# Kernel tuning notes

Measured on AMD Instinct MI355X. Metric: run time of the kernel, lower is better.

## Reference

```python
import jax, jax.numpy as jnp
import numpy as np

# Dimensions
T = 1024      # tokens
D = 1024      # d_model
DFF = 1024    # expert intermediate dim
R = 64        # tucker rank (r_in == r_out)
G = 8         # n_group
E = 32        # experts_per_group
NEXP = G * E  # 256 routed experts
K = 8         # top-k


def setup_inputs() -> dict:
    key = jax.random.key(0)
    ks = jax.random.split(key, 12)
    s = 0.02
    return {
        "x": jax.random.normal(ks[0], (T, D), jnp.float32),
        "Wg": jax.random.normal(ks[1], (D, NEXP), jnp.float32) * s,
        "uin_gate": jax.random.normal(ks[2], (G, D, R), jnp.float32) * s,
        "core_gate": jax.random.normal(ks[3], (G, E, R, R), jnp.float32) * s,
        "uout_gate": jax.random.normal(ks[4], (G, R, DFF), jnp.float32) * s,
        "uin_up": jax.random.normal(ks[5], (G, D, R), jnp.float32) * s,
        "core_up": jax.random.normal(ks[6], (G, E, R, R), jnp.float32) * s,
        "uout_up": jax.random.normal(ks[7], (G, R, DFF), jnp.float32) * s,
        "uin_down": jax.random.normal(ks[8], (G, DFF, R), jnp.float32) * s,
        "core_down": jax.random.normal(ks[9], (G, E, R, R), jnp.float32) * s,
        "uout_down": jax.random.normal(ks[10], (G, R, D), jnp.float32) * s,
    }


def _moe_forward(x, Wg, uin_gate, core_gate, uout_gate,
                 uin_up, core_up, uout_up,
                 uin_down, core_down, uout_down):
    Tn, d = x.shape
    # Router: top-k over 256 experts, softmax over the k logits (fp32 as in torch)
    logits = x @ Wg                                   # [T, NEXP]
    w, sel = jax.lax.top_k(logits, K)                 # [T, K]
    w = jax.nn.softmax(w.astype(jnp.float32), axis=-1).astype(x.dtype)

    e = sel.reshape(-1)                               # [F] global expert id
    g = e // E                                        # [F] group id
    tok = jnp.repeat(jnp.arange(Tn), K)               # [F] source token id
    mask = (g[:, None] == jnp.arange(G)[None, :]).astype(x.dtype)  # [F, G]

    def gather_in(uin):
        # project tokens with every group's u_in once, then gather per pair
        pre = jnp.einsum('td,gdr->gtr', x, uin)       # [G, T, R]
        return pre[g, tok]                            # [F, R]

    def core_apply(xin, core):
        # per-pair Tucker core slice bmm: x.unsqueeze(1) @ core[rel_idx]
        slices = core.reshape(G * E, R, R)[e]         # [F, R, R] gather
        return jnp.einsum('fr,fro->fo', xin, slices)  # [F, R]

    def group_out(h, U):
        # per-pair group-specific projection: h[f] @ U[g_f]
        out = jnp.zeros((h.shape[0], U.shape[-1]), h.dtype)
        for gi in range(G):  # fixed small loop over 8 groups
            out = out + (h * mask[:, gi:gi + 1]) @ U[gi]
        return out

    gate_h = group_out(core_apply(gather_in(uin_gate), core_gate), uout_gate)  # [F, DFF]
    up_h = group_out(core_apply(gather_in(uin_up), core_up), uout_up)          # [F, DFF]
    act = jax.nn.silu(gate_h) * up_h                                           # SwiGLU
    xin_d = group_out(act, uin_down)                                           # [F, R]
    out_f = group_out(core_apply(xin_d, core_down), uout_down)                 # [F, D]
    out_f = out_f * w.reshape(-1)[:, None]
    # scatter-add expert outputs back to tokens
    return jax.ops.segment_sum(out_f, tok, num_segments=Tn)


def reference(x, Wg, uin_gate, core_gate, uout_gate,
              uin_up, core_up, uout_up,
              uin_down, core_down, uout_down):
    return _moe_forward(x, Wg, uin_gate, core_gate, uout_gate,
                        uin_up, core_up, uout_up,
                        uin_down, core_down, uout_down)
```

## Files before the change

### kernel.cpp

```cpp
#include <hip/hip_runtime.h>
#include <hip/hip_bf16.h>
#include <math.h>


#define T_ 1024
#define D_ 1024
#define DFF_ 1024
#define R_ 64
#define G_ 8
#define E_ 32
#define NEXP_ 256
#define K_ 8
#define F_ 8192
#define LKZ_ 4
#define LTB_ 8
#define PKZ_ 2
#define DKZ_ 4

typedef short bf16x8 __attribute__((ext_vector_type(8)));
typedef float f32x4 __attribute__((ext_vector_type(4)));

__device__ __forceinline__ unsigned short f2bf(float f) {
  unsigned int u = __float_as_uint(f);
  u += 0x7fffu + ((u >> 16) & 1u);
  return (unsigned short)(u >> 16);
}

typedef const __attribute__((address_space(1))) unsigned int guint;
typedef __attribute__((address_space(3))) unsigned int luint;

__device__ __forceinline__ void gstage(short* lds, const unsigned short* src,
                                       int gp, int tid) {
  int w = tid >> 6, l = tid & 63;
  int r0 = (w << 4) + (l >> 3);
  int c = (l & 7) << 3;
  __builtin_amdgcn_global_load_lds((guint*)&src[(size_t)r0 * gp + c],
                                   (luint*)&lds[w << 10], 16, 0, 0);
  __builtin_amdgcn_global_load_lds((guint*)&src[(size_t)(r0 + 8) * gp + c],
                                   (luint*)&lds[(w << 10) + 512], 16, 0, 0);
}

__device__ __forceinline__ void gstage_clamp(short* lds, const unsigned short* src,
                                             int gp, int rows_valid, int tid) {
  int w = tid >> 6, l = tid & 63;
  int c = (l & 7) << 3;
  int r0 = (w << 4) + (l >> 3);
  int r1 = r0 + 8;
  if (r0 >= rows_valid) r0 = rows_valid - 1;
  if (r1 >= rows_valid) r1 = rows_valid - 1;
  __builtin_amdgcn_global_load_lds((guint*)&src[(size_t)r0 * gp + c],
                                   (luint*)&lds[w << 10], 16, 0, 0);
  __builtin_amdgcn_global_load_lds((guint*)&src[(size_t)r1 * gp + c],
                                   (luint*)&lds[(w << 10) + 512], 16, 0, 0);
}

__device__ __forceinline__ void mma_strip(const short* As, const short* Bs,
                                          int ms, int lane, f32x4* acc) {
  int lm = lane & 15;
  int lk = (lane >> 4) << 3;
#pragma unroll
  for (int kc = 0; kc < 64; kc += 32) {
    bf16x8 a = *(const bf16x8*)&As[(ms + lm) * 64 + kc + lk];
#pragma unroll
    for (int nt = 0; nt < 4; ++nt) {
      bf16x8 b = *(const bf16x8*)&Bs[(nt * 16 + lm) * 64 + kc + lk];
      acc[nt] = __builtin_amdgcn_mfma_f32_16x16x32_bf16(a, b, acc[nt], 0, 0, 0);
    }
  }
}

__device__ __forceinline__ void a_load(float4* pre, const float* src, int gp, int tid) {
  int r = tid >> 2, c = (tid & 3) << 4;
  const float* s = &src[(size_t)r * gp + c];
  pre[0] = *(const float4*)(s + 0);
  pre[1] = *(const float4*)(s + 4);
  pre[2] = *(const float4*)(s + 8);
  pre[3] = *(const float4*)(s + 12);
}

__device__ __forceinline__ void a_write(short* dst, const float4* pre, int tid) {
  int r = tid >> 2, c = (tid & 3) << 4;
  uint4 u0, u1;
  u0.x = ((unsigned)f2bf(pre[0].y) << 16) | f2bf(pre[0].x);
  u0.y = ((unsigned)f2bf(pre[0].w) << 16) | f2bf(pre[0].z);
  u0.z = ((unsigned)f2bf(pre[1].y) << 16) | f2bf(pre[1].x);
  u0.w = ((unsigned)f2bf(pre[1].w) << 16) | f2bf(pre[1].z);
  u1.x = ((unsigned)f2bf(pre[2].y) << 16) | f2bf(pre[2].x);
  u1.y = ((unsigned)f2bf(pre[2].w) << 16) | f2bf(pre[2].z);
  u1.z = ((unsigned)f2bf(pre[3].y) << 16) | f2bf(pre[3].x);
  u1.w = ((unsigned)f2bf(pre[3].w) << 16) | f2bf(pre[3].z);
  *(uint4*)&dst[r * 64 + c] = u0;
  *(uint4*)&dst[r * 64 + c + 8] = u1;
}

__global__ __launch_bounds__(256) void k_prep_logits(
    const float* __restrict__ x, const float* __restrict__ Wg,
    const float* __restrict__ s0, const float* __restrict__ s1,
    const float* __restrict__ s2, const float* __restrict__ s3,
    const float* __restrict__ s4, const float* __restrict__ s5,
    unsigned short* __restrict__ xb,
    unsigned short* __restrict__ d0, unsigned short* __restrict__ d1,
    unsigned short* __restrict__ d2, unsigned short* __restrict__ d3,
    unsigned short* __restrict__ d4, unsigned short* __restrict__ d5,
    int* __restrict__ cnt, int* __restrict__ tickets, float* __restrict__ Yf,
    float* __restrict__ lp) {
  __shared__ float shbuf[64 * 65];
  int b = blockIdx.x;
  if (b < 512) {
    int t0 = (b & 127) * LTB_;
    int z = b >> 7;
    int e = threadIdx.x;
    float* xs = shbuf;
    float a[LTB_] = {};
    int dc = z * 256;
    {
      int idx = threadIdx.x * 8;
      int tl = idx >> 8, d = idx & 255;
      *(float4*)&xs[tl * 256 + d] = *(const float4*)&x[(size_t)(t0 + tl) * D_ + dc + d];
      *(float4*)&xs[tl * 256 + d + 4] = *(const float4*)&x[(size_t)(t0 + tl) * D_ + dc + d + 4];
    }
    __syncthreads();
#pragma unroll 2
    for (int d2 = 0; d2 < 256; d2 += 4) {
      float w0 = Wg[(size_t)(dc + d2 + 0) * NEXP_ + e];
      float w1 = Wg[(size_t)(dc + d2 + 1) * NEXP_ + e];
      float w2 = Wg[(size_t)(dc + d2 + 2) * NEXP_ + e];
      float w3 = Wg[(size_t)(dc + d2 + 3) * NEXP_ + e];
#pragma unroll
      for (int j = 0; j < LTB_; ++j) {
        float4 xv = *(const float4*)&xs[j * 256 + d2];
        float aj = a[j];
        aj = fmaf(xv.x, w0, aj);
        aj = fmaf(xv.y, w1, aj);
        aj = fmaf(xv.z, w2, aj);
        aj = fmaf(xv.w, w3, aj);
        a[j] = aj;
      }
    }
    size_t base = (size_t)z * T_ * NEXP_;
#pragma unroll
    for (int j = 0; j < LTB_; ++j)
      lp[base + (size_t)(t0 + j) * NEXP_ + e] = a[j];
    return;
  }
  int b2 = b - 512;
  int id = b2 >> 7, rem = b2 & 127, g = rem >> 4, tile = rem & 15;
  if (id == 6) {
    size_t base = ((size_t)g * 16 + tile) * 8192;
    for (int i = threadIdx.x; i < 2048; i += 256) {
      size_t idx = base + (size_t)i * 4;
      float4 v = *(const float4*)&x[idx];
      xb[idx + 0] = f2bf(v.x);
      xb[idx + 1] = f2bf(v.y);
      xb[idx + 2] = f2bf(v.z);
      xb[idx + 3] = f2bf(v.w);
    }
    size_t ybase = ((size_t)g * 16 + tile) * 4096;
    float4 z4 = make_float4(0.f, 0.f, 0.f, 0.f);
    for (int i = threadIdx.x; i < 1024; i += 256)
      *(float4*)&Yf[ybase + (size_t)i * 4] = z4;
    if (g == 0 && tile == 0) {
      cnt[threadIdx.x] = 0;
      if (threadIdx.x == 0) tickets[0] = 0;
    }
    return;
  }
  const float* src = id == 0 ? s0 : id == 1 ? s1 : id == 2 ? s2 : id == 3 ? s3 : id == 4 ? s4 : s5;
  unsigned short* dst = id == 0 ? d0 : id == 1 ? d1 : id == 2 ? d2 : id == 3 ? d3 : id == 4 ? d4 : d5;
  if (id < 3) {
    int r0 = tile * 64;
    for (int idx = threadIdx.x; idx < 4096; idx += 256) {
      int r = idx >> 6, c = idx & 63;
      shbuf[r * 65 + c] = src[((size_t)g * 1024 + r0 + r) * 64 + c];
    }
    __syncthreads();
    for (int idx = threadIdx.x; idx < 4096; idx += 256) {
      int c = idx >> 6, r = idx & 63;
      dst[((size_t)g * 64 + c) * 1024 + r0 + r] = f2bf(shbuf[r * 65 + c]);
    }
  } else {
    int c0 = tile * 64;
    for (int idx = threadIdx.x; idx < 4096; idx += 256) {
      int r = idx >> 6, c = idx & 63;
      shbuf[r * 65 + c] = src[((size_t)g * 64 + r) * 1024 + c0 + c];
    }
    __syncthreads();
    if (id == 5) {
      for (int idx = threadIdx.x; idx < 4096; idx += 256) {
        int c = idx >> 6, r = idx & 63;
        dst[(size_t)(c0 + c) * 512 + g * 64 + r] = f2bf(shbuf[r * 65 + c]);
      }
    } else {
      for (int idx = threadIdx.x; idx < 4096; idx += 256) {
        int c = idx >> 6, r = idx & 63;
        dst[((size_t)g * 1024 + c0 + c) * 64 + r] = f2bf(shbuf[r * 65 + c]);
      }
    }
  }
}

__global__ __launch_bounds__(256) void k_pre_topk(
    const unsigned short* __restrict__ xb,
    const unsigned short* __restrict__ uinT_g, const unsigned short* __restrict__ uinT_u,
    const float* __restrict__ lp,
    float* __restrict__ Pgp, float* __restrict__ Pup,
    float* __restrict__ wsm, int* __restrict__ bucket, int* __restrict__ cnt,
    int* __restrict__ tickets, int* __restrict__ off) {
  __shared__ __align__(16) short sh[4][4096];
  __shared__ int lastfl;
  int b = blockIdx.x;
  int tid = threadIdx.x;
  if (b >= 256) {
    int b2 = b - 256;
    int tile = b2 & 15, g = (b2 >> 4) & 7, zz = b2 >> 7;
    int gu = zz >> 1, kz = zz & 1;
    const unsigned short* U = gu ? uinT_u : uinT_g;
    float* P = gu ? Pup : Pgp;
    int t0 = tile * 64;
    int lane = tid & 63, ms = (tid >> 6) * 16;
    f32x4 acc[4] = {};
    int dlo = kz * (D_ / PKZ_);
    const unsigned short* Asrc = xb + (size_t)t0 * D_;
    const unsigned short* Bsrc = U + (size_t)g * 64 * 1024;
    gstage(sh[0], Asrc + dlo, D_, tid);
    gstage(sh[2], Bsrc + dlo, 1024, tid);
    __syncthreads();
    int cur = 0;
#pragma unroll 1
    for (int i = 0; i < 8; ++i) {
      if (i < 7) {
        int dc = dlo + (i + 1) * 64;
        gstage(sh[cur ^ 1], Asrc + dc, D_, tid);
        gstage(sh[2 + (cur ^ 1)], Bsrc + dc, 1024, tid);
      }
      mma_strip(sh[cur], sh[2 + cur], ms, lane, acc);
      __syncthreads();
      cur ^= 1;
    }
    int lm = lane & 15, lq = (lane >> 4) * 4;
#pragma unroll
    for (int nt = 0; nt < 4; ++nt)
#pragma unroll
      for (int r = 0; r < 4; ++r)
        P[((size_t)(kz * G_ + g) * T_ + t0 + ms + lq + r) * R_ + nt * 16 + lm] = acc[nt][r];
    return;
  }
  int wave = tid >> 6;
  int lane = tid & 63;
  int t = b * 4 + wave;
  float v[4];
  int idx[4];
#pragma unroll
  for (int j = 0; j < 4; ++j) {
    idx[j] = lane + 64 * j;
    float s = 0.f;
#pragma unroll
    for (int z = 0; z < LKZ_; ++z)
      s += lp[(size_t)z * T_ * NEXP_ + (size_t)t * NEXP_ + idx[j]];
    v[j] = s;
  }
  float topv[K_];
  int topi[K_];
#pragma unroll
  for (int k = 0; k < K_; ++k) {
    float bv = v[0];
    int bi = idx[0];
#pragma unroll
    for (int j = 1; j < 4; ++j)
      if (v[j] > bv || (v[j] == bv && idx[j] < bi)) { bv = v[j]; bi = idx[j]; }
#pragma unroll
    for (int o2 = 32; o2 > 0; o2 >>= 1) {
      float ov = __shfl_xor(bv, o2);
      int oi = __shfl_xor(bi, o2);
      if (ov > bv || (ov == bv && oi < bi)) { bv = ov; bi = oi; }
    }
    topv[k] = bv;
    topi[k] = bi;
#pragma unroll
    for (int j = 0; j < 4; ++j)
      if (idx[j] == bi) v[j] = -INFINITY;
  }
  float m = topv[0];
  float ev[K_];
  float s = 0.f;
#pragma unroll
  for (int k = 0; k < K_; ++k) { ev[k] = expf(topv[k] - m); s += ev[k]; }
  float inv = 1.f / s;
  if (lane < K_) {
    wsm[t * K_ + lane] = ev[lane] * inv;
    int r1 = atomicAdd(&cnt[topi[lane]], 1);
    bucket[topi[lane] * 1024 + r1] = t * K_ + lane;
  }
  __threadfence();
  __syncthreads();
  if (tid == 0) lastfl = (atomicAdd(&tickets[0], 1) == 255) ? 1 : 0;
  __syncthreads();
  if (lastfl) {
    int* sarr = (int*)sh;
    int i = tid;
    int c0 = atomicAdd(&cnt[i], 0);
    sarr[i] = c0;
    __syncthreads();
    for (int d = 1; d < NEXP_; d <<= 1) {
      int vv = (i >= d) ? sarr[i - d] : 0;
      __syncthreads();
      sarr[i] += vv;
      __syncthreads();
    }
    off[i + 1] = sarr[i];
    if (i == 0) off[0] = 0;
  }
}

__global__ __launch_bounds__(256) void k_core_gu(const float* __restrict__ Pgp,
                                                 const float* __restrict__ Pup,
                                                 const float* __restrict__ core_g,
                                                 const float* __restrict__ core_u,
                                                 const int* __restrict__ bucket,
                                                 const int* __restrict__ off,
                                                 unsigned short* __restrict__ xgb,
                                                 unsigned short* __restrict__ xub) {
  int e = blockIdx.x >> 1, half = blockIdx.x & 1;
  int g = e >> 5;
  __shared__ float cg[4096], cu[4096];
  __shared__ float rg[4][64], ru[4][64];
  int tid = threadIdx.x;
  for (int i = tid; i < 1024; i += 256) {
    *(float4*)&cg[i * 4] = *(const float4*)&core_g[(size_t)e * 4096 + (size_t)i * 4];
    *(float4*)&cu[i * 4] = *(const float4*)&core_u[(size_t)e * 4096 + (size_t)i * 4];
  }
  int p0 = off[e], n = off[e + 1] - p0;
  if (n < 0) n = 0;
  if (n > 1024) n = 1024;
  int hn = (n + 1) >> 1;
  int i0 = half * hn;
  int i1 = i0 + hn; if (i1 > n) i1 = n;
  int pl = tid >> 6, o = tid & 63;
  __syncthreads();
  for (int ib = i0; ib < i1; ib += 4) {
    int i = ib + pl;
    bool valid = i < i1;
    int p = p0 + i;
    float sg = 0.f, su = 0.f;
    if (valid) {
      int t = bucket[e * 1024 + i] >> 3;
#pragma unroll
      for (int kz = 0; kz < PKZ_; ++kz) {
        sg += Pgp[((size_t)(kz * G_ + g) * T_ + t) * R_ + o];
        su += Pup[((size_t)(kz * G_ + g) * T_ + t) * R_ + o];
      }
    }
    __syncthreads();
    rg[pl][o] = sg;
    ru[pl][o] = su;
    __syncthreads();
    if (valid) {
      float ag = 0.f, au = 0.f;
#pragma unroll 8
      for (int r = 0; r < R_; ++r) {
        ag = fmaf(rg[pl][r], cg[r * R_ + o], ag);
        au = fmaf(ru[pl][r], cu[r * R_ + o], au);
      }
      xgb[(size_t)p * R_ + o] = f2bf(ag);
      xub[(size_t)p * R_ + o] = f2bf(au);
    }
  }
}

__global__ __launch_bounds__(256) void k_fused_ad(const unsigned short* __restrict__ xgb,
                                                  const unsigned short* __restrict__ xub,
                                                  const unsigned short* __restrict__ uoutT_g,
                                                  const unsigned short* __restrict__ uoutT_u,
                                                  const unsigned short* __restrict__ uinT_d,
                                                  const int* __restrict__ off,
                                                  float* __restrict__ xdp) {
  int g = blockIdx.y;
  int kz = blockIdx.z;
  int p0 = off[g * E_];
  int pend = off[g * E_ + E_];
  if (p0 < 0) p0 = 0;
  if (pend > F_) pend = F_;
  if (pend < p0) pend = p0;
  int ntiles = (pend - p0 + 63) >> 6;
  __shared__ __align__(16) short Ag[4096], Au[4096], Pt[4096];
  __shared__ __align__(16) short Bg[2][4096], Bu[2][4096], Bd[2][4096];
  int tid = threadIdx.x, lane = tid & 63, ms = (tid >> 6) * 16;
  int lm = lane & 15, lq = (lane >> 4) * 4;
  int cc0 = kz * (DFF_ / DKZ_);
  const unsigned short* Bgsrc = uoutT_g + (size_t)g * DFF_ * R_;
  const unsigned short* Busrc = uoutT_u + (size_t)g * DFF_ * R_;
  const unsigned short* Bdsrc = uinT_d + (size_t)g * 64 * 1024;
  for (int tile = blockIdx.x; tile < ntiles; tile += gridDim.x) {
    int pbase = p0 + tile * 64;
    int rv = pend - pbase; if (rv > 64) rv = 64;
    gstage_clamp(Ag, xgb + (size_t)pbase * R_, R_, rv, tid);
    gstage_clamp(Au, xub + (size_t)pbase * R_, R_, rv, tid);
    gstage(Bg[0], Bgsrc + (size_t)cc0 * R_, R_, tid);
    gstage(Bu[0], Busrc + (size_t)cc0 * R_, R_, tid);
    gstage(Bd[0], Bdsrc + cc0, 1024, tid);
    __syncthreads();
    f32x4 accd[4] = {};
    int cur = 0;
#pragma unroll 1
    for (int c4 = 0; c4 < 4; ++c4) {
      if (c4 < 3) {
        int cc = cc0 + (c4 + 1) * 64;
        gstage(Bg[cur ^ 1], Bgsrc + (size_t)cc * R_, R_, tid);
        gstage(Bu[cur ^ 1], Busrc + (size_t)cc * R_, R_, tid);
        gstage(Bd[cur ^ 1], Bdsrc + cc, 1024, tid);
      }
      f32x4 accg[4] = {}, accu[4] = {};
      mma_strip(Ag, Bg[cur], ms, lane, accg);
      mma_strip(Au, Bu[cur], ms, lane, accu);
#pragma unroll
      for (int nt = 0; nt < 4; ++nt)
#pragma unroll
        for (int r = 0; r < 4; ++r) {
          float gv = accg[nt][r];
          float av = gv / (1.f + expf(-gv)) * accu[nt][r];
          Pt[(ms + lq + r) * 64 + nt * 16 + lm] = (short)f2bf(av);
        }
      mma_strip(Pt, Bd[cur], ms, lane, accd);
      __syncthreads();
      cur ^= 1;
    }
#pragma unroll
    for (int nt = 0; nt < 4; ++nt)
#pragma unroll
      for (int r = 0; r < 4; ++r) {
        int p = pbase + ms + lq + r;
        if (p < pend) xdp[((size_t)kz * F_ + p) * R_ + nt * 16 + lm] = accd[nt][r];
      }
    __syncthreads();
  }
}

__global__ __launch_bounds__(256) void k_down_core(const float* __restrict__ xdp,
                                                   const float* __restrict__ core_d,
                                                   const int* __restrict__ bucket,
                                                   const float* __restrict__ wsm,
                                                   const int* __restrict__ off,
                                                   float* __restrict__ Yf) {
  int e = blockIdx.x >> 1, half = blockIdx.x & 1;
  int g = e >> 5;
  __shared__ float cd[4096];
  __shared__ float xs[4][64];
  int tid = threadIdx.x;
  for (int i = tid; i < 1024; i += 256)
    *(float4*)&cd[i * 4] = *(const float4*)&core_d[(size_t)e * 4096 + (size_t)i * 4];
  int p0 = off[e], n = off[e + 1] - p0;
  if (n < 0) n = 0;
  if (n > 1024) n = 1024;
  int hn = (n + 1) >> 1;
  int i0 = half * hn;
  int i1 = i0 + hn; if (i1 > n) i1 = n;
  int pl = tid >> 6, o = tid & 63;
  __syncthreads();
  for (int ib = i0; ib < i1; ib += 4) {
    int i = ib + pl;
    bool valid = i < i1;
    int p = p0 + i;
    int f = valid ? bucket[e * 1024 + i] : 0;
    float s = 0.f;
    if (valid) {
#pragma unroll
      for (int kz = 0; kz < DKZ_; ++kz) s += xdp[((size_t)kz * F_ + p) * R_ + o];
    }
    __syncthreads();
    xs[pl][o] = s;
    __syncthreads();
    if (valid) {
      float a = 0.f;
#pragma unroll 8
      for (int r = 0; r < R_; ++r) a = fmaf(xs[pl][r], cd[r * R_ + o], a);
      atomicAdd(&Yf[(size_t)(f >> 3) * 512 + g * 64 + o], wsm[f] * a);
    }
  }
}

__global__ __launch_bounds__(256) void k_fin(const float* __restrict__ Yf,
                                             const unsigned short* __restrict__ Uod2T,
                                             float* __restrict__ out) {
  int t0 = blockIdx.x * 64;
  int d0 = blockIdx.y * 64;
  __shared__ __align__(16) short sh[4][4096];
  int tid = threadIdx.x, lane = tid & 63, ms = (tid >> 6) * 16;
  int lm = lane & 15, lq = (lane >> 4) * 4;
  const float* Asrc = Yf + (size_t)t0 * 512;
  const unsigned short* Bsrc = Uod2T + (size_t)d0 * 512;
  f32x4 acc[4] = {};
  {
    float4 pre[4];
    a_load(pre, Asrc, 512, tid);
    a_write(sh[0], pre, tid);
  }
  gstage(sh[2], Bsrc, 512, tid);
  __syncthreads();
  int cur = 0;
#pragma unroll 1
  for (int i = 0; i < 8; ++i) {
    float4 pre[4];
    bool hp = i < 7;
    if (hp) {
      int kc = (i + 1) * 64;
      a_load(pre, Asrc + kc, 512, tid);
      gstage(sh[2 + (cur ^ 1)], Bsrc + kc, 512, tid);
    }
    mma_strip(sh[cur], sh[2 + cur], ms, lane, acc);
    if (hp) a_write(sh[cur ^ 1], pre, tid);
    __syncthreads();
    cur ^= 1;
  }
  float* Os = (float*)sh;
#pragma unroll
  for (int nt = 0; nt < 4; ++nt)
#pragma unroll
    for (int r = 0; r < 4; ++r)
      Os[(ms + lq + r) * 68 + nt * 16 + lm] = acc[nt][r];
  __syncthreads();
  for (int idx = tid; idx < 1024; idx += 256) {
    int r = idx >> 4, c4 = (idx & 15) << 2;
    *(float4*)&out[(size_t)(t0 + r) * D_ + d0 + c4] = *(const float4*)&Os[r * 68 + c4];
  }
}

extern "C" void kernel_launch(void* const* d_in, const int* in_sizes, int n_in,
                              void* d_out, int out_size, void* d_ws, size_t ws_size,
                              hipStream_t stream) {
  const float* x = (const float*)d_in[0];
  const float* Wg = (const float*)d_in[1];
  const float* uin_gate = (const float*)d_in[2];
  const float* core_gate = (const float*)d_in[3];
  const float* uout_gate = (const float*)d_in[4];
  const float* uin_up = (const float*)d_in[5];
  const float* core_up = (const float*)d_in[6];
  const float* uout_up = (const float*)d_in[7];
  const float* uin_down = (const float*)d_in[8];
  const float* core_down = (const float*)d_in[9];
  const float* uout_down = (const float*)d_in[10];
  float* out = (float*)d_out;

  char* ws = (char*)d_ws;
  size_t o = 0;
  auto alloc = [&](size_t bytes) { size_t r = o; o = (o + bytes + 255) & ~(size_t)255; return r; };
  size_t o_lp = alloc((size_t)LKZ_ * T_ * NEXP_ * 4);
  size_t o_wsm = alloc(F_ * 4);
  size_t o_bucket = alloc((size_t)NEXP_ * 1024 * 4);
  size_t o_cnt = alloc(NEXP_ * 4);
  size_t o_tickets = alloc(256);
  size_t o_off = alloc((NEXP_ + 1) * 4);
  size_t o_xb = alloc((size_t)T_ * D_ * 2);
  size_t o_uinT_g = alloc((size_t)G_ * 64 * 1024 * 2);
  size_t o_uinT_u = alloc((size_t)G_ * 64 * 1024 * 2);
  size_t o_uinT_d = alloc((size_t)G_ * 64 * 1024 * 2);
  size_t o_uoutT_g = alloc((size_t)G_ * 1024 * 64 * 2);
  size_t o_uoutT_u = alloc((size_t)G_ * 1024 * 64 * 2);
  size_t o_Uod2T = alloc((size_t)D_ * 512 * 2);
  size_t o_xgb = alloc((size_t)F_ * R_ * 2);
  size_t o_xub = alloc((size_t)F_ * R_ * 2);
  size_t o_Y = alloc((size_t)T_ * 512 * 4);
  size_t o_pgp = alloc((size_t)PKZ_ * G_ * T_ * R_ * 4);
  size_t o_pup = alloc((size_t)PKZ_ * G_ * T_ * R_ * 4);
  size_t o_xdp = alloc((size_t)DKZ_ * F_ * R_ * 4);
  (void)ws_size;

  float* lp = (float*)(ws + o_lp);
  float* wsm = (float*)(ws + o_wsm);
  int* bucket = (int*)(ws + o_bucket);
  int* cnt = (int*)(ws + o_cnt);
  int* tickets = (int*)(ws + o_tickets);
  int* off = (int*)(ws + o_off);
  unsigned short* xb = (unsigned short*)(ws + o_xb);
  unsigned short* uinT_g = (unsigned short*)(ws + o_uinT_g);
  unsigned short* uinT_u = (unsigned short*)(ws + o_uinT_u);
  unsigned short* uinT_d = (unsigned short*)(ws + o_uinT_d);
  unsigned short* uoutT_g = (unsigned short*)(ws + o_uoutT_g);
  unsigned short* uoutT_u = (unsigned short*)(ws + o_uoutT_u);
  unsigned short* Uod2T = (unsigned short*)(ws + o_Uod2T);
  unsigned short* xgb = (unsigned short*)(ws + o_xgb);
  unsigned short* xub = (unsigned short*)(ws + o_xub);
  float* Yf = (float*)(ws + o_Y);
  float* pgp = (float*)(ws + o_pgp);
  float* pup = (float*)(ws + o_pup);
  float* xdp = (float*)(ws + o_xdp);

  k_prep_logits<<<1408, 256, 0, stream>>>(x, Wg, uin_gate, uin_up, uin_down,
                                          uout_gate, uout_up, uout_down, xb,
                                          uinT_g, uinT_u, uinT_d,
                                          uoutT_g, uoutT_u, Uod2T,
                                          cnt, tickets, Yf, lp);
  k_pre_topk<<<768, 256, 0, stream>>>(xb, uinT_g, uinT_u, lp, pgp, pup,
                                      wsm, bucket, cnt, tickets, off);
  k_core_gu<<<NEXP_ * 2, 256, 0, stream>>>(pgp, pup, core_gate, core_up, bucket, off, xgb, xub);
  k_fused_ad<<<dim3(16, G_, DKZ_), 256, 0, stream>>>(xgb, xub, uoutT_g, uoutT_u, uinT_d, off, xdp);
  k_down_core<<<NEXP_ * 2, 256, 0, stream>>>(xdp, core_down, bucket, wsm, off, Yf);
  k_fin<<<dim3(16, 16), 256, 0, stream>>>(Yf, Uod2T, out);
}
```

Before: 222.7 us.

## XOR-swizzle LDS tiles for MFMA reads and split pre-projection from top-k kernel

Applies an XOR swizzle on 16-byte chunks to every LDS tile: global_load_lds sources are permuted, a_write and the SiLU product tile writes are permuted, and MFMA fragment reads de-permute. The aim is to remove LDS bank conflicts on the row-strided bf16x8 reads. It also splits the combined projection+topk kernel into two launches, which frees the top-k kernel from the large shared buffer at the cost of one extra launch.

```diff
diff --git a/kernel.cpp b/kernel.cpp
--- a/kernel.cpp
+++ b/kernel.cpp
@@ -29,41 +29,44 @@
 typedef const __attribute__((address_space(1))) unsigned int guint;
 typedef __attribute__((address_space(3))) unsigned int luint;
 
-__device__ __forceinline__ void gstage(short* lds, const unsigned short* src,
-                                       int gp, int tid) {
+__device__ __forceinline__ void gstage_swz(short* lds, const unsigned short* src,
+                                           int gp, int tid) {
   int w = tid >> 6, l = tid & 63;
-  int r0 = (w << 4) + (l >> 3);
-  int c = (l & 7) << 3;
-  __builtin_amdgcn_global_load_lds((guint*)&src[(size_t)r0 * gp + c],
+  int rs = (w << 4) + (l >> 3);
+  int cs = ((l & 7) ^ (rs & 7)) << 3;
+  __builtin_amdgcn_global_load_lds((guint*)&src[(size_t)rs * gp + cs],
                                    (luint*)&lds[w << 10], 16, 0, 0);
-  __builtin_amdgcn_global_load_lds((guint*)&src[(size_t)(r0 + 8) * gp + c],
+  __builtin_amdgcn_global_load_lds((guint*)&src[(size_t)(rs + 8) * gp + cs],
                                    (luint*)&lds[(w << 10) + 512], 16, 0, 0);
 }
 
-__device__ __forceinline__ void gstage_clamp(short* lds, const unsigned short* src,
-                                             int gp, int rows_valid, int tid) {
+__device__ __forceinline__ void gstage_clamp_swz(short* lds, const unsigned short* src,
+                                                 int gp, int rows_valid, int tid) {
   int w = tid >> 6, l = tid & 63;
-  int c = (l & 7) << 3;
-  int r0 = (w << 4) + (l >> 3);
-  int r1 = r0 + 8;
+  int rs = (w << 4) + (l >> 3);
+  int cs = ((l & 7) ^ (rs & 7)) << 3;
+  int r0 = rs, r1 = rs + 8;
   if (r0 >= rows_valid) r0 = rows_valid - 1;
   if (r1 >= rows_valid) r1 = rows_valid - 1;
-  __builtin_amdgcn_global_load_lds((guint*)&src[(size_t)r0 * gp + c],
+  __builtin_amdgcn_global_load_lds((guint*)&src[(size_t)r0 * gp + cs],
                                    (luint*)&lds[w << 10], 16, 0, 0);
-  __builtin_amdgcn_global_load_lds((guint*)&src[(size_t)r1 * gp + c],
+  __builtin_amdgcn_global_load_lds((guint*)&src[(size_t)r1 * gp + cs],
                                    (luint*)&lds[(w << 10) + 512], 16, 0, 0);
 }
 
-__device__ __forceinline__ void mma_strip(const short* As, const short* Bs,
-                                          int ms, int lane, f32x4* acc) {
+__device__ __forceinline__ void mma_strip_swz(const short* As, const short* Bs,
+                                              int ms, int lane, f32x4* acc) {
   int lm = lane & 15;
   int lk = (lane >> 4) << 3;
+  int x7 = lm & 7;
 #pragma unroll
   for (int kc = 0; kc < 64; kc += 32) {
-    bf16x8 a = *(const bf16x8*)&As[(ms + lm) * 64 + kc + lk];
+    int ch = (kc + lk) >> 3;
+    int co = ((ch ^ x7) << 3);
+    bf16x8 a = *(const bf16x8*)&As[(ms + lm) * 64 + co];
 #pragma unroll
     for (int nt = 0; nt < 4; ++nt) {
-      bf16x8 b = *(const bf16x8*)&Bs[(nt * 16 + lm) * 64 + kc + lk];
+      bf16x8 b = *(const bf16x8*)&Bs[(nt * 16 + lm) * 64 + co];
       acc[nt] = __builtin_amdgcn_mfma_f32_16x16x32_bf16(a, b, acc[nt], 0, 0, 0);
     }
   }
@@ -78,8 +81,9 @@
   pre[3] = *(const float4*)(s + 12);
 }
 
-__device__ __forceinline__ void a_write(short* dst, const float4* pre, int tid) {
-  int r = tid >> 2, c = (tid & 3) << 4;
+__device__ __forceinline__ void a_write_swz(short* dst, const float4* pre, int tid) {
+  int r = tid >> 2;
+  int ch0 = (tid & 3) << 1;
   uint4 u0, u1;
   u0.x = ((unsigned)f2bf(pre[0].y) << 16) | f2bf(pre[0].x);
   u0.y = ((unsigned)f2bf(pre[0].w) << 16) | f2bf(pre[0].z);
@@ -89,8 +93,9 @@
   u1.y = ((unsigned)f2bf(pre[2].w) << 16) | f2bf(pre[2].z);
   u1.z = ((unsigned)f2bf(pre[3].y) << 16) | f2bf(pre[3].x);
   u1.w = ((unsigned)f2bf(pre[3].w) << 16) | f2bf(pre[3].z);
-  *(uint4*)&dst[r * 64 + c] = u0;
-  *(uint4*)&dst[r * 64 + c + 8] = u1;
+  int r7 = r & 7;
+  *(uint4*)&dst[r * 64 + ((ch0 ^ r7) << 3)] = u0;
+  *(uint4*)&dst[r * 64 + (((ch0 + 1) ^ r7) << 3)] = u1;
 }
 
 __global__ __launch_bounds__(256) void k_prep_logits(
@@ -199,52 +204,54 @@
   }
 }
 
-__global__ __launch_bounds__(256) void k_pre_topk(
+__global__ __launch_bounds__(256) void k_pre(
     const unsigned short* __restrict__ xb,
     const unsigned short* __restrict__ uinT_g, const unsigned short* __restrict__ uinT_u,
+    float* __restrict__ Pgp, float* __restrict__ Pup) {
+  __shared__ __align__(16) short sh[4][4096];
+  int b = blockIdx.x;
+  int tid = threadIdx.x;
+  int tile = b & 15, g = (b >> 4) & 7, zz = b >> 7;
+  int gu = zz >> 1, kz = zz & 1;
+  const unsigned short* U = gu ? uinT_u : uinT_g;
+  float* P = gu ? Pup : Pgp;
+  int t0 = tile * 64;
+  int lane = tid & 63, ms = (tid >> 6) * 16;
+  f32x4 acc[4] = {};
+  int dlo = kz * (D_ / PKZ_);
+  const unsigned short* Asrc = xb + (size_t)t0 * D_;
+  const unsigned short* Bsrc = U + (size_t)g * 64 * 1024;
+  gstage_swz(sh[0], Asrc + dlo, D_, tid);
+  gstage_swz(sh[2], Bsrc + dlo, 1024, tid);
+  __syncthreads();
+  int cur = 0;
+#pragma unroll 1
+  for (int i = 0; i < 8; ++i) {
+    if (i < 7) {
+      int dc = dlo + (i + 1) * 64;
+      gstage_swz(sh[cur ^ 1], Asrc + dc, D_, tid);
+      gstage_swz(sh[2 + (cur ^ 1)], Bsrc + dc, 1024, tid);
+    }
+    mma_strip_swz(sh[cur], sh[2 + cur], ms, lane, acc);
+    __syncthreads();
+    cur ^= 1;
+  }
+  int lm = lane & 15, lq = (lane >> 4) * 4;
+#pragma unroll
+  for (int nt = 0; nt < 4; ++nt)
+#pragma unroll
+    for (int r = 0; r < 4; ++r)
+      P[((size_t)(kz * G_ + g) * T_ + t0 + ms + lq + r) * R_ + nt * 16 + lm] = acc[nt][r];
+}
+
+__global__ __launch_bounds__(256) void k_topk(
     const float* __restrict__ lp,
-    float* __restrict__ Pgp, float* __restrict__ Pup,
     float* __restrict__ wsm, int* __restrict__ bucket, int* __restrict__ cnt,
     int* __restrict__ tickets, int* __restrict__ off) {
-  __shared__ __align__(16) short sh[4][4096];
+  __shared__ int sarr[NEXP_];
   __shared__ int lastfl;
   int b = blockIdx.x;
   int tid = threadIdx.x;
-  if (b >= 256) {
-    int b2 = b - 256;
-    int tile = b2 & 15, g = (b2 >> 4) & 7, zz = b2 >> 7;
-    int gu = zz >> 1, kz = zz & 1;
-    const unsigned short* U = gu ? uinT_u : uinT_g;
-    float* P = gu ? Pup : Pgp;
-    int t0 = tile * 64;
-    int lane = tid & 63, ms = (tid >> 6) * 16;
-    f32x4 acc[4] = {};
-    int dlo = kz * (D_ / PKZ_);
-    const unsigned short* Asrc = xb + (size_t)t0 * D_;
-    const unsigned short* Bsrc = U + (size_t)g * 64 * 1024;
-    gstage(sh[0], Asrc + dlo, D_, tid);
-    gstage(sh[2], Bsrc + dlo, 1024, tid);
-    __syncthreads();
-    int cur = 0;
-#pragma unroll 1
-    for (int i = 0; i < 8; ++i) {
-      if (i < 7) {
-        int dc = dlo + (i + 1) * 64;
-        gstage(sh[cur ^ 1], Asrc + dc, D_, tid);
-        gstage(sh[2 + (cur ^ 1)], Bsrc + dc, 1024, tid);
-      }
-      mma_strip(sh[cur], sh[2 + cur], ms, lane, acc);
-      __syncthreads();
-      cur ^= 1;
-    }
-    int lm = lane & 15, lq = (lane >> 4) * 4;
-#pragma unroll
-    for (int nt = 0; nt < 4; ++nt)
-#pragma unroll
-      for (int r = 0; r < 4; ++r)
-        P[((size_t)(kz * G_ + g) * T_ + t0 + ms + lq + r) * R_ + nt * 16 + lm] = acc[nt][r];
-    return;
-  }
   int wave = tid >> 6;
   int lane = tid & 63;
   int t = b * 4 + wave;
@@ -296,7 +303,6 @@
   if (tid == 0) lastfl = (atomicAdd(&tickets[0], 1) == 255) ? 1 : 0;
   __syncthreads();
   if (lastfl) {
-    int* sarr = (int*)sh;
     int i = tid;
     int c0 = atomicAdd(&cnt[i], 0);
     sarr[i] = c0;
@@ -393,11 +399,11 @@
   for (int tile = blockIdx.x; tile < ntiles; tile += gridDim.x) {
     int pbase = p0 + tile * 64;
     int rv = pend - pbase; if (rv > 64) rv = 64;
-    gstage_clamp(Ag, xgb + (size_t)pbase * R_, R_, rv, tid);
-    gstage_clamp(Au, xub + (size_t)pbase * R_, R_, rv, tid);
-    gstage(Bg[0], Bgsrc + (size_t)cc0 * R_, R_, tid);
-    gstage(Bu[0], Busrc + (size_t)cc0 * R_, R_, tid);
-    gstage(Bd[0], Bdsrc + cc0, 1024, tid);
+    gstage_clamp_swz(Ag, xgb + (size_t)pbase * R_, R_, rv, tid);
+    gstage_clamp_swz(Au, xub + (size_t)pbase * R_, R_, rv, tid);
+    gstage_swz(Bg[0], Bgsrc + (size_t)cc0 * R_, R_, tid);
+    gstage_swz(Bu[0], Busrc + (size_t)cc0 * R_, R_, tid);
+    gstage_swz(Bd[0], Bdsrc + cc0, 1024, tid);
     __syncthreads();
     f32x4 accd[4] = {};
     int cur = 0;
@@ -405,22 +411,24 @@
     for (int c4 = 0; c4 < 4; ++c4) {
       if (c4 < 3) {
         int cc = cc0 + (c4 + 1) * 64;
-        gstage(Bg[cur ^ 1], Bgsrc + (size_t)cc * R_, R_, tid);
-        gstage(Bu[cur ^ 1], Busrc + (size_t)cc * R_, R_, tid);
-        gstage(Bd[cur ^ 1], Bdsrc + cc, 1024, tid);
+        gstage_swz(Bg[cur ^ 1], Bgsrc + (size_t)cc * R_, R_, tid);
+        gstage_swz(Bu[cur ^ 1], Busrc + (size_t)cc * R_, R_, tid);
+        gstage_swz(Bd[cur ^ 1], Bdsrc + cc, 1024, tid);
       }
       f32x4 accg[4] = {}, accu[4] = {};
-      mma_strip(Ag, Bg[cur], ms, lane, accg);
-      mma_strip(Au, Bu[cur], ms, lane, accu);
+      mma_strip_swz(Ag, Bg[cur], ms, lane, accg);
+      mma_strip_swz(Au, Bu[cur], ms, lane, accu);
 #pragma unroll
       for (int nt = 0; nt < 4; ++nt)
 #pragma unroll
         for (int r = 0; r < 4; ++r) {
           float gv = accg[nt][r];
           float av = gv / (1.f + expf(-gv)) * accu[nt][r];
-          Pt[(ms + lq + r) * 64 + nt * 16 + lm] = (short)f2bf(av);
+          int prow = ms + lq + r;
+          int pch = (nt << 1) + (lm >> 3);
+          Pt[prow * 64 + ((pch ^ (prow & 7)) << 3) + (lm & 7)] = (short)f2bf(av);
         }
-      mma_strip(Pt, Bd[cur], ms, lane, accd);
+      mma_strip_swz(Pt, Bd[cur], ms, lane, accd);
       __syncthreads();
       cur ^= 1;
     }
@@ -492,9 +500,9 @@
   {
     float4 pre[4];
     a_load(pre, Asrc, 512, tid);
-    a_write(sh[0], pre, tid);
-  }
-  gstage(sh[2], Bsrc, 512, tid);
+    a_write_swz(sh[0], pre, tid);
+  }
+  gstage_swz(sh[2], Bsrc, 512, tid);
   __syncthreads();
   int cur = 0;
 #pragma unroll 1
@@ -504,10 +512,10 @@
     if (hp) {
       int kc = (i + 1) * 64;
       a_load(pre, Asrc + kc, 512, tid);
-      gstage(sh[2 + (cur ^ 1)], Bsrc + kc, 512, tid);
-    }
-    mma_strip(sh[cur], sh[2 + cur], ms, lane, acc);
-    if (hp) a_write(sh[cur ^ 1], pre, tid);
+      gstage_swz(sh[2 + (cur ^ 1)], Bsrc + kc, 512, tid);
+    }
+    mma_strip_swz(sh[cur], sh[2 + cur], ms, lane, acc);
+    if (hp) a_write_swz(sh[cur ^ 1], pre, tid);
     __syncthreads();
     cur ^= 1;
   }
@@ -589,8 +597,8 @@
                                           uinT_g, uinT_u, uinT_d,
                                           uoutT_g, uoutT_u, Uod2T,
                                           cnt, tickets, Yf, lp);
-  k_pre_topk<<<768, 256, 0, stream>>>(xb, uinT_g, uinT_u, lp, pgp, pup,
-                                      wsm, bucket, cnt, tickets, off);
+  k_pre<<<512, 256, 0, stream>>>(xb, uinT_g, uinT_u, pgp, pup);
+  k_topk<<<256, 256, 0, stream>>>(lp, wsm, bucket, cnt, tickets, off);
   k_core_gu<<<NEXP_ * 2, 256, 0, stream>>>(pgp, pup, core_gate, core_up, bucket, off, xgb, xub);
   k_fused_ad<<<dim3(16, G_, DKZ_), 256, 0, stream>>>(xgb, xub, uoutT_g, uoutT_u, uinT_d, off, xdp);
   k_down_core<<<NEXP_ * 2, 256, 0, stream>>>(xdp, core_down, bucket, wsm, off, Yf);
```

After: 210.4 us. 1.06x faster.
